# Kernel tuning notes

Hardware: AMD Instinct MI355X
Metric: run time of the kernel (lower is better)

The kernel has to match this reference:

```python
import jax, jax.numpy as jnp
import numpy as np

N_NODES = 50000
SEQ_LEN = 32
N_TOKENS = 100000
EMB_DIM = 128          # in_feats / 2
IN_FEATS = 256
N_HIDDEN = 256
N_CLASSES = 40
N_EDGES = 800000
PAD_IX = 0


def setup_inputs() -> dict:
    key = jax.random.key(0)
    k1, k2, k3, k4, k5, k6 = jax.random.split(key, 6)
    features = jax.random.randint(k1, (N_NODES, SEQ_LEN), 0, N_TOKENS, dtype=jnp.int32)
    src = jax.random.randint(k2, (N_EDGES,), 0, N_NODES, dtype=jnp.int32)
    dst = jax.random.randint(k3, (N_EDGES,), 0, N_NODES, dtype=jnp.int32)
    emb_table = jax.random.normal(k4, (N_TOKENS, EMB_DIM), dtype=jnp.float32) * 0.02
    W1 = jax.random.normal(k5, (IN_FEATS, N_HIDDEN), dtype=jnp.float32) * 0.02
    b1 = jnp.zeros((N_HIDDEN,), dtype=jnp.float32)
    W2 = jax.random.normal(k6, (N_HIDDEN, N_CLASSES), dtype=jnp.float32) * 0.02
    b2 = jnp.zeros((N_CLASSES,), dtype=jnp.float32)
    return {"features": features, "src": src, "dst": dst,
            "emb_table": emb_table, "W1": W1, "b1": b1, "W2": W2, "b2": b2}


def _apply_embs(features, emb_table):
    # padding_idx row contributes zeros (nn.Embedding padding_idx semantics)
    emb = emb_table.at[PAD_IX].set(0.0)
    h = emb[features]                                    # [N, L, D]
    seq_len = jnp.sum(features != PAD_IX, axis=1)        # [N]
    seq_len = jnp.maximum(seq_len, 1)[:, None].astype(h.dtype)
    h1 = h.sum(axis=1) / seq_len                         # masked mean
    h2 = h.max(axis=1)                                   # max pool (pads are 0)
    return jnp.concatenate((h1, h2), axis=1)             # [N, 2D]


def _graph_conv(h, src, dst, norm_s, norm_d, W, b):
    # DGL GraphConv, norm='both': out = D_in^{-1/2} A D_out^{-1/2} h W + b
    hw = h @ W                                           # transform first (smaller msgs)
    m = (hw * norm_s[:, None])[src]                      # gather messages [E, F]
    agg = jax.ops.segment_sum(m, dst, num_segments=N_NODES)
    return agg * norm_d[:, None] + b


def reference(features, src, dst, emb_table, W1, b1, W2, b2):
    ones_e = jnp.ones((src.shape[0],), dtype=jnp.float32)
    deg_out = jnp.maximum(jax.ops.segment_sum(ones_e, src, num_segments=N_NODES), 1.0)
    deg_in = jnp.maximum(jax.ops.segment_sum(ones_e, dst, num_segments=N_NODES), 1.0)
    norm_s = deg_out ** -0.5
    norm_d = deg_in ** -0.5

    h = _apply_embs(features, emb_table)                 # [N, in_feats]
    h = jax.nn.relu(_graph_conv(h, src, dst, norm_s, norm_d, W1, b1))
    # dropout is identity in eval mode
    h = _graph_conv(h, src, dst, norm_s, norm_d, W2, b2)
    return h                                             # [N, n_classes]
```

## Files before the change

kernel.cpp:

```cpp
#include <hip/hip_runtime.h>
#include <math.h>

#define N_NODES 50000
#define SEQ_LEN 32
#define EMB_DIM 128
#define IN_FEATS 256
#define N_HIDDEN 256
#define N_CLASSES 40
#define N_EDGES 800000
#define N_TOKENS 100000

#define SLOT 64
#define NBIN 196
#define BINCAP 4608
#define EPB 4000

typedef short short8 __attribute__((ext_vector_type(8)));
typedef float f32x4 __attribute__((ext_vector_type(4)));

__device__ __forceinline__ unsigned short f2bf(float x) {
  unsigned int u = __float_as_uint(x);
  unsigned int r = (u + 0x7FFFu + ((u >> 16) & 1u)) >> 16;
  return (unsigned short)r;
}
__device__ __forceinline__ float bf2f(unsigned short s) {
  return __uint_as_float((unsigned int)s << 16);
}
__device__ __forceinline__ unsigned int pack2bf(float a, float b) {
  return (unsigned int)f2bf(a) | ((unsigned int)f2bf(b) << 16);
}

__global__ __launch_bounds__(256) void k_pre(const int* __restrict__ src,
                                             const int* __restrict__ dst,
                                             int* __restrict__ gcntD,
                                             int* __restrict__ gcntS,
                                             unsigned int* __restrict__ dbin,
                                             unsigned char* __restrict__ sbin,
                                             const float* __restrict__ emb,
                                             unsigned short* __restrict__ emb_b,
                                             const float* __restrict__ W1,
                                             unsigned short* __restrict__ Wp1,
                                             const float* __restrict__ W2,
                                             unsigned short* __restrict__ Wp2) {
  __shared__ int cntD[NBIN], cntS[NBIN], baseD[NBIN], baseS[NBIN];
  int b = blockIdx.x, tid = threadIdx.x;
  if (b < 200) {
    if (tid < NBIN) { cntD[tid] = 0; cntS[tid] = 0; }
    __syncthreads();
    int e0 = b * EPB;
    for (int j = tid; j < EPB; j += 256) {
      int d = dst[e0 + j], s = src[e0 + j];
      atomicAdd(&cntD[d >> 8], 1);
      atomicAdd(&cntS[s >> 8], 1);
    }
    __syncthreads();
    if (tid < NBIN) {
      baseD[tid] = atomicAdd(&gcntD[tid], cntD[tid]);
      baseS[tid] = atomicAdd(&gcntS[tid], cntS[tid]);
      cntD[tid] = 0;
      cntS[tid] = 0;
    }
    __syncthreads();
    for (int j = tid; j < EPB; j += 256) {
      int d = dst[e0 + j], s = src[e0 + j];
      int bd = d >> 8, bs = s >> 8;
      int od = atomicAdd(&cntD[bd], 1);
      int pd = baseD[bd] + od;
      if (pd < BINCAP) dbin[(size_t)bd * BINCAP + pd] = ((unsigned int)s << 8) | (unsigned int)(d & 255);
      int os = atomicAdd(&cntS[bs], 1);
      int ps = baseS[bs] + os;
      if (ps < BINCAP) sbin[(size_t)bs * BINCAP + ps] = (unsigned char)(s & 255);
    }
  } else if (b < 200 + 2048) {
    const int total = N_TOKENS * EMB_DIM / 4;
    for (int i = (b - 200) * 256 + tid; i < total; i += 2048 * 256) {
      float4 v = ((const float4*)emb)[i];
      ushort4 o;
      o.x = f2bf(v.x); o.y = f2bf(v.y); o.z = f2bf(v.z); o.w = f2bf(v.w);
      ((ushort4*)emb_b)[i] = o;
    }
  } else if (b < 200 + 2048 + 32) {
    int g = (b - 2248) * 256 + tid;
    int lane = g & 63, jb = (g >> 6) & 15, kt = g >> 10;
    int col = jb * 16 + (lane & 15);
    int kbase = kt * 32 + (lane >> 4) * 8;
    unsigned short* o = Wp1 + (size_t)g * 8;
    #pragma unroll
    for (int e = 0; e < 8; ++e) o[e] = f2bf(W1[(size_t)(kbase + e) * N_HIDDEN + col]);
  } else {
    int g = (b - 2280) * 256 + tid;
    if (g < 8 * 3 * 64) {
      int lane = g & 63, jb = (g >> 6) % 3, kt = g / (3 * 64);
      int col = jb * 16 + (lane & 15);
      int kbase = kt * 32 + (lane >> 4) * 8;
      unsigned short* o = Wp2 + (size_t)g * 8;
      #pragma unroll
      for (int e = 0; e < 8; ++e)
        o[e] = (col < N_CLASSES) ? f2bf(W2[(size_t)(kbase + e) * N_CLASSES + col]) : (unsigned short)0;
    }
  }
}

__global__ __launch_bounds__(256) void k_graph2(const unsigned int* __restrict__ dbin,
                                                const int* __restrict__ gcntD,
                                                const unsigned char* __restrict__ sbin,
                                                const int* __restrict__ gcntS,
                                                int* __restrict__ cursor,
                                                int* __restrict__ csr_pad,
                                                float* __restrict__ norm_s,
                                                float* __restrict__ norm_d) {
  __shared__ int cntD[256], cntS[256];
  int tid = threadIdx.x, b = blockIdx.x;
  cntD[tid] = 0; cntS[tid] = 0;
  __syncthreads();
  int n = min(gcntD[b], BINCAP);
  const unsigned int* bb = dbin + (size_t)b * BINCAP;
  for (int j = tid; j < n; j += 256) {
    unsigned int e = bb[j];
    int lo = e & 255;
    int slot = atomicAdd(&cntD[lo], 1);
    if (slot < SLOT) csr_pad[(size_t)(b * 256 + lo) * SLOT + slot] = (int)(e >> 8);
  }
  int ns = min(gcntS[b], BINCAP);
  const unsigned char* sb = sbin + (size_t)b * BINCAP;
  for (int j = tid; j < ns; j += 256) atomicAdd(&cntS[sb[j]], 1);
  __syncthreads();
  int node = b * 256 + tid;
  if (node < N_NODES) {
    cursor[node] = min(cntD[tid], SLOT);
    norm_d[node] = 1.0f / sqrtf((float)max(cntD[tid], 1));
    norm_s[node] = 1.0f / sqrtf((float)max(cntS[tid], 1));
  }
}

__global__ __launch_bounds__(512) void k_emb_mm1(const int* __restrict__ feats,
                                                 const uint4* __restrict__ rows4,
                                                 const unsigned short* __restrict__ Wp,
                                                 unsigned short* __restrict__ out) {
  __shared__ unsigned short sA[64 * 256];
  int tid = threadIdx.x;
  int w = tid >> 6, lane = tid & 63;
  int r0 = blockIdx.x * 64;
  int lq = lane & 15, qg = lane >> 4, laneL = lane & 31;

  #pragma unroll
  for (int n = 0; n < 8; ++n) {
    int r = w * 8 + n;
    int node = r0 + r;
    int tok0 = 0;
    if (node < N_NODES) tok0 = feats[(size_t)node * SEQ_LEN + laneL];
    unsigned long long m = __ballot(tok0 != 0);
    int cnt = (int)__popcll(m & 0xFFFFFFFFull);
    float inv = 1.0f / (float)max(cnt, 1);

    float s0 = 0.f, s1 = 0.f, s2 = 0.f, s3 = 0.f, s4 = 0.f, s5 = 0.f, s6 = 0.f, s7 = 0.f;
    float m0 = 0.f, m1 = 0.f, m2 = 0.f, m3 = 0.f, m4 = 0.f, m5 = 0.f, m6 = 0.f, m7 = 0.f;
    bool first = true;
    #pragma unroll
    for (int t = 0; t < 8; ++t) {
      int tok = __shfl(tok0, t * 4 + qg);
      uint4 v = make_uint4(0u, 0u, 0u, 0u);
      if (tok) v = rows4[(size_t)tok * 16 + lq];
      float f0 = bf2f((unsigned short)(v.x & 0xFFFF)), f1 = bf2f((unsigned short)(v.x >> 16));
      float f2 = bf2f((unsigned short)(v.y & 0xFFFF)), f3 = bf2f((unsigned short)(v.y >> 16));
      float f4 = bf2f((unsigned short)(v.z & 0xFFFF)), f5 = bf2f((unsigned short)(v.z >> 16));
      float f6 = bf2f((unsigned short)(v.w & 0xFFFF)), f7 = bf2f((unsigned short)(v.w >> 16));
      s0 += f0; s1 += f1; s2 += f2; s3 += f3; s4 += f4; s5 += f5; s6 += f6; s7 += f7;
      if (first) { m0 = f0; m1 = f1; m2 = f2; m3 = f3; m4 = f4; m5 = f5; m6 = f6; m7 = f7; first = false; }
      else {
        m0 = fmaxf(m0, f0); m1 = fmaxf(m1, f1); m2 = fmaxf(m2, f2); m3 = fmaxf(m3, f3);
        m4 = fmaxf(m4, f4); m5 = fmaxf(m5, f5); m6 = fmaxf(m6, f6); m7 = fmaxf(m7, f7);
      }
    }
    #pragma unroll
    for (int mask = 16; mask <= 32; mask <<= 1) {
      s0 += __shfl_xor(s0, mask); s1 += __shfl_xor(s1, mask);
      s2 += __shfl_xor(s2, mask); s3 += __shfl_xor(s3, mask);
      s4 += __shfl_xor(s4, mask); s5 += __shfl_xor(s5, mask);
      s6 += __shfl_xor(s6, mask); s7 += __shfl_xor(s7, mask);
      m0 = fmaxf(m0, __shfl_xor(m0, mask)); m1 = fmaxf(m1, __shfl_xor(m1, mask));
      m2 = fmaxf(m2, __shfl_xor(m2, mask)); m3 = fmaxf(m3, __shfl_xor(m3, mask));
      m4 = fmaxf(m4, __shfl_xor(m4, mask)); m5 = fmaxf(m5, __shfl_xor(m5, mask));
      m6 = fmaxf(m6, __shfl_xor(m6, mask)); m7 = fmaxf(m7, __shfl_xor(m7, mask));
    }
    if (qg == 0) {
      int kb1 = lq, kb2 = 16 + lq;
      *(uint4*)&sA[r * 256 + ((kb1 ^ (r & 7)) << 3)] =
          make_uint4(pack2bf(s0 * inv, s1 * inv), pack2bf(s2 * inv, s3 * inv),
                     pack2bf(s4 * inv, s5 * inv), pack2bf(s6 * inv, s7 * inv));
      *(uint4*)&sA[r * 256 + ((kb2 ^ (r & 7)) << 3)] =
          make_uint4(pack2bf(m0, m1), pack2bf(m2, m3), pack2bf(m4, m5), pack2bf(m6, m7));
    }
  }
  __syncthreads();

  const short8* W8 = (const short8*)Wp;
  f32x4 acc[4][2];
  #pragma unroll
  for (int i = 0; i < 4; ++i) { acc[i][0] = (f32x4){0.f,0.f,0.f,0.f}; acc[i][1] = (f32x4){0.f,0.f,0.f,0.f}; }

  #pragma unroll
  for (int kt = 0; kt < 8; ++kt) {
    short8 a[4];
    int kb = kt * 4 + (lane >> 4);
    #pragma unroll
    for (int ri = 0; ri < 4; ++ri) {
      int r = ri * 16 + (lane & 15);
      a[ri] = *(const short8*)&sA[r * 256 + ((kb ^ (r & 7)) << 3)];
    }
    short8 b0 = W8[(kt * 16 + w * 2 + 0) * 64 + lane];
    short8 b1 = W8[(kt * 16 + w * 2 + 1) * 64 + lane];
    #pragma unroll
    for (int ri = 0; ri < 4; ++ri) {
      acc[ri][0] = __builtin_amdgcn_mfma_f32_16x16x32_bf16(a[ri], b0, acc[ri][0], 0, 0, 0);
      acc[ri][1] = __builtin_amdgcn_mfma_f32_16x16x32_bf16(a[ri], b1, acc[ri][1], 0, 0, 0);
    }
  }

  #pragma unroll
  for (int ri = 0; ri < 4; ++ri) {
    #pragma unroll
    for (int rr = 0; rr < 4; ++rr) {
      int row = r0 + ri * 16 + (lane >> 4) * 4 + rr;
      if (row < N_NODES) {
        #pragma unroll
        for (int jb = 0; jb < 2; ++jb) {
          int col = w * 32 + jb * 16 + (lane & 15);
          out[(size_t)row * 256 + col] = f2bf(acc[ri][jb][rr]);
        }
      }
    }
  }
}

__global__ __launch_bounds__(512) void k_agg_mm2(const uint4* __restrict__ rows4,
                                                 const int* __restrict__ cursor,
                                                 const int* __restrict__ csr_pad,
                                                 const float* __restrict__ norm_s,
                                                 const float* __restrict__ norm_d,
                                                 const float* __restrict__ b1,
                                                 const unsigned short* __restrict__ Wp,
                                                 unsigned short* __restrict__ out) {
  __shared__ unsigned short sA[64 * 256];
  int tid = threadIdx.x;
  int w = tid >> 6, lane = tid & 63;
  int r0 = blockIdx.x * 64;
  int half = lane >> 5, lq = lane & 31;

  #pragma unroll
  for (int n = 0; n < 8; ++n) {
    int r = w * 8 + n;
    int node = r0 + r;
    float a0 = 0.f, a1 = 0.f, a2 = 0.f, a3 = 0.f, a4 = 0.f, a5 = 0.f, a6 = 0.f, a7 = 0.f;
    if (node < N_NODES) {
      int cnt = __builtin_amdgcn_readfirstlane(cursor[node]);
      const int* csr = csr_pad + (size_t)node * SLOT;
      int e = 0;
      for (; e + 8 <= cnt; e += 8) {
        int s0 = csr[e + 0 + half], s1 = csr[e + 2 + half];
        int s2 = csr[e + 4 + half], s3 = csr[e + 6 + half];
        float ns0 = norm_s[s0], ns1 = norm_s[s1], ns2 = norm_s[s2], ns3 = norm_s[s3];
        uint4 v0 = rows4[(size_t)s0 * 32 + lq];
        uint4 v1 = rows4[(size_t)s1 * 32 + lq];
        uint4 v2 = rows4[(size_t)s2 * 32 + lq];
        uint4 v3 = rows4[(size_t)s3 * 32 + lq];
        #pragma unroll
        for (int i = 0; i < 4; ++i) {
          uint4 v = (i == 0) ? v0 : (i == 1) ? v1 : (i == 2) ? v2 : v3;
          float ns = (i == 0) ? ns0 : (i == 1) ? ns1 : (i == 2) ? ns2 : ns3;
          a0 += ns * bf2f((unsigned short)(v.x & 0xFFFF)); a1 += ns * bf2f((unsigned short)(v.x >> 16));
          a2 += ns * bf2f((unsigned short)(v.y & 0xFFFF)); a3 += ns * bf2f((unsigned short)(v.y >> 16));
          a4 += ns * bf2f((unsigned short)(v.z & 0xFFFF)); a5 += ns * bf2f((unsigned short)(v.z >> 16));
          a6 += ns * bf2f((unsigned short)(v.w & 0xFFFF)); a7 += ns * bf2f((unsigned short)(v.w >> 16));
        }
      }
      for (; e + 2 <= cnt; e += 2) {
        int s = csr[e + half];
        float ns = norm_s[s];
        uint4 v = rows4[(size_t)s * 32 + lq];
        a0 += ns * bf2f((unsigned short)(v.x & 0xFFFF)); a1 += ns * bf2f((unsigned short)(v.x >> 16));
        a2 += ns * bf2f((unsigned short)(v.y & 0xFFFF)); a3 += ns * bf2f((unsigned short)(v.y >> 16));
        a4 += ns * bf2f((unsigned short)(v.z & 0xFFFF)); a5 += ns * bf2f((unsigned short)(v.z >> 16));
        a6 += ns * bf2f((unsigned short)(v.w & 0xFFFF)); a7 += ns * bf2f((unsigned short)(v.w >> 16));
      }
      if (e < cnt && half == 0) {
        int s = csr[e];
        float ns = norm_s[s];
        uint4 v = rows4[(size_t)s * 32 + lq];
        a0 += ns * bf2f((unsigned short)(v.x & 0xFFFF)); a1 += ns * bf2f((unsigned short)(v.x >> 16));
        a2 += ns * bf2f((unsigned short)(v.y & 0xFFFF)); a3 += ns * bf2f((unsigned short)(v.y >> 16));
        a4 += ns * bf2f((unsigned short)(v.z & 0xFFFF)); a5 += ns * bf2f((unsigned short)(v.z >> 16));
        a6 += ns * bf2f((unsigned short)(v.w & 0xFFFF)); a7 += ns * bf2f((unsigned short)(v.w >> 16));
      }
    }
    a0 += __shfl_xor(a0, 32); a1 += __shfl_xor(a1, 32);
    a2 += __shfl_xor(a2, 32); a3 += __shfl_xor(a3, 32);
    a4 += __shfl_xor(a4, 32); a5 += __shfl_xor(a5, 32);
    a6 += __shfl_xor(a6, 32); a7 += __shfl_xor(a7, 32);

    if (half == 0) {
      float nd = (node < N_NODES) ? norm_d[node] : 1.0f;
      float4 bb0 = *(const float4*)&b1[8 * lq];
      float4 bb1 = *(const float4*)&b1[8 * lq + 4];
      float o0 = fmaxf(a0 * nd + bb0.x, 0.f), o1 = fmaxf(a1 * nd + bb0.y, 0.f);
      float o2 = fmaxf(a2 * nd + bb0.z, 0.f), o3 = fmaxf(a3 * nd + bb0.w, 0.f);
      float o4 = fmaxf(a4 * nd + bb1.x, 0.f), o5 = fmaxf(a5 * nd + bb1.y, 0.f);
      float o6 = fmaxf(a6 * nd + bb1.z, 0.f), o7 = fmaxf(a7 * nd + bb1.w, 0.f);
      *(uint4*)&sA[r * 256 + ((lq ^ (r & 7)) << 3)] =
          make_uint4(pack2bf(o0, o1), pack2bf(o2, o3), pack2bf(o4, o5), pack2bf(o6, o7));
    }
  }
  __syncthreads();

  if (w < 4) {
    const short8* W8 = (const short8*)Wp;
    f32x4 acc[3];
    #pragma unroll
    for (int j = 0; j < 3; ++j) acc[j] = (f32x4){0.f, 0.f, 0.f, 0.f};
    #pragma unroll
    for (int kt = 0; kt < 8; ++kt) {
      int r = w * 16 + (lane & 15);
      int kb = kt * 4 + (lane >> 4);
      short8 a = *(const short8*)&sA[r * 256 + ((kb ^ (r & 7)) << 3)];
      #pragma unroll
      for (int jb = 0; jb < 3; ++jb) {
        short8 b = W8[(kt * 3 + jb) * 64 + lane];
        acc[jb] = __builtin_amdgcn_mfma_f32_16x16x32_bf16(a, b, acc[jb], 0, 0, 0);
      }
    }
    #pragma unroll
    for (int rr = 0; rr < 4; ++rr) {
      int row = r0 + w * 16 + (lane >> 4) * 4 + rr;
      if (row < N_NODES) {
        float ns = norm_s[row];
        #pragma unroll
        for (int jb = 0; jb < 3; ++jb) {
          int col = jb * 16 + (lane & 15);
          if (col < N_CLASSES) out[(size_t)row * N_CLASSES + col] = f2bf(acc[jb][rr] * ns);
        }
      }
    }
  }
}

__global__ __launch_bounds__(256) void k_agg2(const unsigned int* __restrict__ rows,
                                              const int* __restrict__ cursor,
                                              const int* __restrict__ csr_pad,
                                              const float* __restrict__ norm_d,
                                              const float* __restrict__ b2,
                                              float* __restrict__ out) {
  int tid = threadIdx.x;
  int w = tid >> 6, lane = tid & 63;
  int node = blockIdx.x * 4 + w;
  int slot = lane / 20, fl = lane % 20;
  int cnt = __builtin_amdgcn_readfirstlane(cursor[node]);
  const int* csr = csr_pad + (size_t)node * SLOT;

  float a0 = 0.f, a1 = 0.f;
  if (slot < 3) {
    for (int e = slot; e < cnt; e += 3) {
      int s = csr[e];
      unsigned int v = rows[(size_t)s * 20 + fl];
      a0 += bf2f((unsigned short)(v & 0xFFFF));
      a1 += bf2f((unsigned short)(v >> 16));
    }
  }
  float p0 = __shfl(a0, lane + 20), p1 = __shfl(a1, lane + 20);
  float q0 = __shfl(a0, lane + 40), q1 = __shfl(a1, lane + 40);
  if (slot == 0) {
    a0 += p0 + q0; a1 += p1 + q1;
    float nd = norm_d[node];
    float o0 = a0 * nd + b2[2 * fl];
    float o1 = a1 * nd + b2[2 * fl + 1];
    *(float2*)&out[(size_t)node * N_CLASSES + 2 * fl] = make_float2(o0, o1);
  }
}

extern "C" void kernel_launch(void* const* d_in, const int* in_sizes, int n_in,
                              void* d_out, int out_size, void* d_ws, size_t ws_size,
                              hipStream_t stream) {
  const int*   feats = (const int*)d_in[0];
  const int*   src   = (const int*)d_in[1];
  const int*   dst   = (const int*)d_in[2];
  const float* emb   = (const float*)d_in[3];
  const float* W1    = (const float*)d_in[4];
  const float* b1    = (const float*)d_in[5];
  const float* W2    = (const float*)d_in[6];
  const float* b2    = (const float*)d_in[7];
  float* out = (float*)d_out;

  char* base = (char*)d_ws;
  size_t off = 0;
  auto alloc = [&](size_t bytes) -> char* {
    char* p = base + off;
    off += (bytes + 255) & ~(size_t)255;
    return p;
  };
  unsigned short* msgb    = (unsigned short*)alloc((size_t)N_NODES * N_HIDDEN * 2);
  unsigned short* hw2b    = (unsigned short*)alloc((size_t)N_NODES * N_CLASSES * 2);
  unsigned short* emb_b   = (unsigned short*)alloc((size_t)N_TOKENS * EMB_DIM * 2);
  unsigned short* Wp1     = (unsigned short*)alloc((size_t)8 * 16 * 64 * 8 * 2);
  unsigned short* Wp2     = (unsigned short*)alloc((size_t)8 * 3 * 64 * 8 * 2);
  int*   gcnt    = (int*)alloc((size_t)512 * 4);
  int*   gcntD   = gcnt;
  int*   gcntS   = gcnt + 256;
  int*   cursor  = (int*)alloc((size_t)N_NODES * 4);
  float* norm_s  = (float*)alloc((size_t)N_NODES * 4);
  float* norm_d  = (float*)alloc((size_t)N_NODES * 4);
  unsigned int*  dbin = (unsigned int*)alloc((size_t)NBIN * BINCAP * 4);
  unsigned char* sbin = (unsigned char*)alloc((size_t)NBIN * BINCAP);
  int*   csr_pad = (int*)alloc((size_t)N_NODES * SLOT * 4);

  hipMemsetAsync(gcnt, 0, 512 * 4, stream);

  k_pre<<<200 + 2048 + 32 + 6, 256, 0, stream>>>(src, dst, gcntD, gcntS, dbin, sbin,
                                                 emb, emb_b, W1, Wp1, W2, Wp2);
  k_graph2<<<NBIN, 256, 0, stream>>>(dbin, gcntD, sbin, gcntS, cursor, csr_pad, norm_s, norm_d);

  int gemm_blocks = (N_NODES + 63) / 64;
  k_emb_mm1<<<gemm_blocks, 512, 0, stream>>>(feats, (const uint4*)emb_b, Wp1, msgb);
  k_agg_mm2<<<gemm_blocks, 512, 0, stream>>>((const uint4*)msgb, cursor, csr_pad,
                                             norm_s, norm_d, b1, Wp2, hw2b);
  k_agg2<<<N_NODES / 4, 256, 0, stream>>>((const unsigned int*)hw2b, cursor, csr_pad, norm_d, b2, out);
}
```

Measured before the change: 230.8 us.

## Split fused aggregation+GEMM2 into separate kernels and fold norm_s into GEMM1 output

The source-degree normalization moves out of the first aggregation's gather loop and into the epilogue of the first GEMM, so the aggregation no longer does a dependent norm_s lookup per edge. The fused agg+mm2 kernel is split into a one-wave-per-node aggregation kernel that writes the hidden layer to a new bf16 buffer, then a separate GEMM kernel that reads it back. The second aggregation is also widened to 6 edge slots with 8-byte loads per lane. The trade is an extra 25 MB write and read of the hidden activations plus one more launch, in exchange for better occupancy and load balance in the gather.

```diff
diff --git a/kernel.cpp b/kernel.cpp
--- a/kernel.cpp
+++ b/kernel.cpp
@@ -136,6 +136,7 @@
 __global__ __launch_bounds__(512) void k_emb_mm1(const int* __restrict__ feats,
                                                  const uint4* __restrict__ rows4,
                                                  const unsigned short* __restrict__ Wp,
+                                                 const float* __restrict__ norm_s,
                                                  unsigned short* __restrict__ out) {
   __shared__ unsigned short sA[64 * 256];
   int tid = threadIdx.x;
@@ -223,127 +224,133 @@
     for (int rr = 0; rr < 4; ++rr) {
       int row = r0 + ri * 16 + (lane >> 4) * 4 + rr;
       if (row < N_NODES) {
+        float ns = norm_s[row];
         #pragma unroll
         for (int jb = 0; jb < 2; ++jb) {
           int col = w * 32 + jb * 16 + (lane & 15);
-          out[(size_t)row * 256 + col] = f2bf(acc[ri][jb][rr]);
+          out[(size_t)row * 256 + col] = f2bf(acc[ri][jb][rr] * ns);
         }
       }
     }
   }
 }
 
-__global__ __launch_bounds__(512) void k_agg_mm2(const uint4* __restrict__ rows4,
-                                                 const int* __restrict__ cursor,
-                                                 const int* __restrict__ csr_pad,
-                                                 const float* __restrict__ norm_s,
-                                                 const float* __restrict__ norm_d,
-                                                 const float* __restrict__ b1,
-                                                 const unsigned short* __restrict__ Wp,
-                                                 unsigned short* __restrict__ out) {
+__global__ __launch_bounds__(256) void k_agg1(const uint4* __restrict__ rows4,
+                                              const int* __restrict__ cursor,
+                                              const int* __restrict__ csr_pad,
+                                              const float* __restrict__ norm_d,
+                                              const float* __restrict__ b1,
+                                              uint4* __restrict__ out4) {
+  int tid = threadIdx.x;
+  int w = tid >> 6, lane = tid & 63;
+  int node = blockIdx.x * 4 + w;
+  int cnt = __builtin_amdgcn_readfirstlane(cursor[node]);
+  const int* csr = csr_pad + (size_t)node * SLOT;
+  int half = lane >> 5, lq = lane & 31;
+
+  float a0 = 0.f, a1 = 0.f, a2 = 0.f, a3 = 0.f, a4 = 0.f, a5 = 0.f, a6 = 0.f, a7 = 0.f;
+  int e = 0;
+  for (; e + 8 <= cnt; e += 8) {
+    int s0 = csr[e + 0 + half], s1 = csr[e + 2 + half];
+    int s2 = csr[e + 4 + half], s3 = csr[e + 6 + half];
+    uint4 v0 = rows4[(size_t)s0 * 32 + lq];
+    uint4 v1 = rows4[(size_t)s1 * 32 + lq];
+    uint4 v2 = rows4[(size_t)s2 * 32 + lq];
+    uint4 v3 = rows4[(size_t)s3 * 32 + lq];
+    #pragma unroll
+    for (int i = 0; i < 4; ++i) {
+      uint4 v = (i == 0) ? v0 : (i == 1) ? v1 : (i == 2) ? v2 : v3;
+      a0 += bf2f((unsigned short)(v.x & 0xFFFF)); a1 += bf2f((unsigned short)(v.x >> 16));
+      a2 += bf2f((unsigned short)(v.y & 0xFFFF)); a3 += bf2f((unsigned short)(v.y >> 16));
+      a4 += bf2f((unsigned short)(v.z & 0xFFFF)); a5 += bf2f((unsigned short)(v.z >> 16));
+      a6 += bf2f((unsigned short)(v.w & 0xFFFF)); a7 += bf2f((unsigned short)(v.w >> 16));
+    }
+  }
+  for (; e + 2 <= cnt; e += 2) {
+    int s = csr[e + half];
+    uint4 v = rows4[(size_t)s * 32 + lq];
+    a0 += bf2f((unsigned short)(v.x & 0xFFFF)); a1 += bf2f((unsigned short)(v.x >> 16));
+    a2 += bf2f((unsigned short)(v.y & 0xFFFF)); a3 += bf2f((unsigned short)(v.y >> 16));
+    a4 += bf2f((unsigned short)(v.z & 0xFFFF)); a5 += bf2f((unsigned short)(v.z >> 16));
+    a6 += bf2f((unsigned short)(v.w & 0xFFFF)); a7 += bf2f((unsigned short)(v.w >> 16));
+  }
+  if (e < cnt) {
+    uint4 v = make_uint4(0u, 0u, 0u, 0u);
+    if (half == 0) v = rows4[(size_t)csr[e] * 32 + lq];
+    a0 += bf2f((unsigned short)(v.x & 0xFFFF)); a1 += bf2f((unsigned short)(v.x >> 16));
+    a2 += bf2f((unsigned short)(v.y & 0xFFFF)); a3 += bf2f((unsigned short)(v.y >> 16));
+    a4 += bf2f((unsigned short)(v.z & 0xFFFF)); a5 += bf2f((unsigned short)(v.z >> 16));
+    a6 += bf2f((unsigned short)(v.w & 0xFFFF)); a7 += bf2f((unsigned short)(v.w >> 16));
+  }
+  a0 += __shfl_xor(a0, 32); a1 += __shfl_xor(a1, 32);
+  a2 += __shfl_xor(a2, 32); a3 += __shfl_xor(a3, 32);
+  a4 += __shfl_xor(a4, 32); a5 += __shfl_xor(a5, 32);
+  a6 += __shfl_xor(a6, 32); a7 += __shfl_xor(a7, 32);
+
+  if (half == 0) {
+    float nd = norm_d[node];
+    float4 bb0 = *(const float4*)&b1[8 * lq];
+    float4 bb1 = *(const float4*)&b1[8 * lq + 4];
+    float o0 = fmaxf(a0 * nd + bb0.x, 0.f), o1 = fmaxf(a1 * nd + bb0.y, 0.f);
+    float o2 = fmaxf(a2 * nd + bb0.z, 0.f), o3 = fmaxf(a3 * nd + bb0.w, 0.f);
+    float o4 = fmaxf(a4 * nd + bb1.x, 0.f), o5 = fmaxf(a5 * nd + bb1.y, 0.f);
+    float o6 = fmaxf(a6 * nd + bb1.z, 0.f), o7 = fmaxf(a7 * nd + bb1.w, 0.f);
+    out4[(size_t)node * 32 + lq] = make_uint4(pack2bf(o0, o1), pack2bf(o2, o3),
+                                              pack2bf(o4, o5), pack2bf(o6, o7));
+  }
+}
+
+__global__ __launch_bounds__(256) void k_mm2(const unsigned short* __restrict__ h2b,
+                                             const unsigned short* __restrict__ Wp,
+                                             const float* __restrict__ norm_s,
+                                             unsigned short* __restrict__ out) {
   __shared__ unsigned short sA[64 * 256];
   int tid = threadIdx.x;
+  int r0 = blockIdx.x * 64;
+  #pragma unroll
+  for (int it = 0; it < 8; ++it) {
+    int idx = it * 256 + tid;
+    int r = idx >> 5, kb = idx & 31;
+    uint4 v = make_uint4(0, 0, 0, 0);
+    int row = r0 + r;
+    if (row < N_NODES) v = *(const uint4*)(h2b + (size_t)row * 256 + kb * 8);
+    *(uint4*)&sA[r * 256 + ((kb ^ (r & 7)) << 3)] = v;
+  }
+  __syncthreads();
+
   int w = tid >> 6, lane = tid & 63;
-  int r0 = blockIdx.x * 64;
-  int half = lane >> 5, lq = lane & 31;
-
-  #pragma unroll
-  for (int n = 0; n < 8; ++n) {
-    int r = w * 8 + n;
-    int node = r0 + r;
-    float a0 = 0.f, a1 = 0.f, a2 = 0.f, a3 = 0.f, a4 = 0.f, a5 = 0.f, a6 = 0.f, a7 = 0.f;
-    if (node < N_NODES) {
-      int cnt = __builtin_amdgcn_readfirstlane(cursor[node]);
-      const int* csr = csr_pad + (size_t)node * SLOT;
-      int e = 0;
-      for (; e + 8 <= cnt; e += 8) {
-        int s0 = csr[e + 0 + half], s1 = csr[e + 2 + half];
-        int s2 = csr[e + 4 + half], s3 = csr[e + 6 + half];
-        float ns0 = norm_s[s0], ns1 = norm_s[s1], ns2 = norm_s[s2], ns3 = norm_s[s3];
-        uint4 v0 = rows4[(size_t)s0 * 32 + lq];
-        uint4 v1 = rows4[(size_t)s1 * 32 + lq];
-        uint4 v2 = rows4[(size_t)s2 * 32 + lq];
-        uint4 v3 = rows4[(size_t)s3 * 32 + lq];
-        #pragma unroll
-        for (int i = 0; i < 4; ++i) {
-          uint4 v = (i == 0) ? v0 : (i == 1) ? v1 : (i == 2) ? v2 : v3;
-          float ns = (i == 0) ? ns0 : (i == 1) ? ns1 : (i == 2) ? ns2 : ns3;
-          a0 += ns * bf2f((unsigned short)(v.x & 0xFFFF)); a1 += ns * bf2f((unsigned short)(v.x >> 16));
-          a2 += ns * bf2f((unsigned short)(v.y & 0xFFFF)); a3 += ns * bf2f((unsigned short)(v.y >> 16));
-          a4 += ns * bf2f((unsigned short)(v.z & 0xFFFF)); a5 += ns * bf2f((unsigned short)(v.z >> 16));
-          a6 += ns * bf2f((unsigned short)(v.w & 0xFFFF)); a7 += ns * bf2f((unsigned short)(v.w >> 16));
-        }
-      }
-      for (; e + 2 <= cnt; e += 2) {
-        int s = csr[e + half];
-        float ns = norm_s[s];
-        uint4 v = rows4[(size_t)s * 32 + lq];
-        a0 += ns * bf2f((unsigned short)(v.x & 0xFFFF)); a1 += ns * bf2f((unsigned short)(v.x >> 16));
-        a2 += ns * bf2f((unsigned short)(v.y & 0xFFFF)); a3 += ns * bf2f((unsigned short)(v.y >> 16));
-        a4 += ns * bf2f((unsigned short)(v.z & 0xFFFF)); a5 += ns * bf2f((unsigned short)(v.z >> 16));
-        a6 += ns * bf2f((unsigned short)(v.w & 0xFFFF)); a7 += ns * bf2f((unsigned short)(v.w >> 16));
-      }
-      if (e < cnt && half == 0) {
-        int s = csr[e];
-        float ns = norm_s[s];
-        uint4 v = rows4[(size_t)s * 32 + lq];
-        a0 += ns * bf2f((unsigned short)(v.x & 0xFFFF)); a1 += ns * bf2f((unsigned short)(v.x >> 16));
-        a2 += ns * bf2f((unsigned short)(v.y & 0xFFFF)); a3 += ns * bf2f((unsigned short)(v.y >> 16));
-        a4 += ns * bf2f((unsigned short)(v.z & 0xFFFF)); a5 += ns * bf2f((unsigned short)(v.z >> 16));
-        a6 += ns * bf2f((unsigned short)(v.w & 0xFFFF)); a7 += ns * bf2f((unsigned short)(v.w >> 16));
-      }
-    }
-    a0 += __shfl_xor(a0, 32); a1 += __shfl_xor(a1, 32);
-    a2 += __shfl_xor(a2, 32); a3 += __shfl_xor(a3, 32);
-    a4 += __shfl_xor(a4, 32); a5 += __shfl_xor(a5, 32);
-    a6 += __shfl_xor(a6, 32); a7 += __shfl_xor(a7, 32);
-
-    if (half == 0) {
-      float nd = (node < N_NODES) ? norm_d[node] : 1.0f;
-      float4 bb0 = *(const float4*)&b1[8 * lq];
-      float4 bb1 = *(const float4*)&b1[8 * lq + 4];
-      float o0 = fmaxf(a0 * nd + bb0.x, 0.f), o1 = fmaxf(a1 * nd + bb0.y, 0.f);
-      float o2 = fmaxf(a2 * nd + bb0.z, 0.f), o3 = fmaxf(a3 * nd + bb0.w, 0.f);
-      float o4 = fmaxf(a4 * nd + bb1.x, 0.f), o5 = fmaxf(a5 * nd + bb1.y, 0.f);
-      float o6 = fmaxf(a6 * nd + bb1.z, 0.f), o7 = fmaxf(a7 * nd + bb1.w, 0.f);
-      *(uint4*)&sA[r * 256 + ((lq ^ (r & 7)) << 3)] =
-          make_uint4(pack2bf(o0, o1), pack2bf(o2, o3), pack2bf(o4, o5), pack2bf(o6, o7));
-    }
-  }
-  __syncthreads();
-
-  if (w < 4) {
-    const short8* W8 = (const short8*)Wp;
-    f32x4 acc[3];
-    #pragma unroll
-    for (int j = 0; j < 3; ++j) acc[j] = (f32x4){0.f, 0.f, 0.f, 0.f};
-    #pragma unroll
-    for (int kt = 0; kt < 8; ++kt) {
-      int r = w * 16 + (lane & 15);
-      int kb = kt * 4 + (lane >> 4);
-      short8 a = *(const short8*)&sA[r * 256 + ((kb ^ (r & 7)) << 3)];
+  const short8* W8 = (const short8*)Wp;
+  f32x4 acc[3];
+  #pragma unroll
+  for (int j = 0; j < 3; ++j) acc[j] = (f32x4){0.f, 0.f, 0.f, 0.f};
+
+  #pragma unroll
+  for (int kt = 0; kt < 8; ++kt) {
+    int r = w * 16 + (lane & 15);
+    int kb = kt * 4 + (lane >> 4);
+    short8 a = *(const short8*)&sA[r * 256 + ((kb ^ (r & 7)) << 3)];
+    #pragma unroll
+    for (int jb = 0; jb < 3; ++jb) {
+      short8 b = W8[(kt * 3 + jb) * 64 + lane];
+      acc[jb] = __builtin_amdgcn_mfma_f32_16x16x32_bf16(a, b, acc[jb], 0, 0, 0);
+    }
+  }
+
+  #pragma unroll
+  for (int rr = 0; rr < 4; ++rr) {
+    int row = r0 + w * 16 + (lane >> 4) * 4 + rr;
+    if (row < N_NODES) {
+      float ns = norm_s[row];
       #pragma unroll
       for (int jb = 0; jb < 3; ++jb) {
-        short8 b = W8[(kt * 3 + jb) * 64 + lane];
-        acc[jb] = __builtin_amdgcn_mfma_f32_16x16x32_bf16(a, b, acc[jb], 0, 0, 0);
+        int col = jb * 16 + (lane & 15);
+        if (col < N_CLASSES) out[(size_t)row * N_CLASSES + col] = f2bf(acc[jb][rr] * ns);
       }
     }
-    #pragma unroll
-    for (int rr = 0; rr < 4; ++rr) {
-      int row = r0 + w * 16 + (lane >> 4) * 4 + rr;
-      if (row < N_NODES) {
-        float ns = norm_s[row];
-        #pragma unroll
-        for (int jb = 0; jb < 3; ++jb) {
-          int col = jb * 16 + (lane & 15);
-          if (col < N_CLASSES) out[(size_t)row * N_CLASSES + col] = f2bf(acc[jb][rr] * ns);
-        }
-      }
-    }
-  }
-}
-
-__global__ __launch_bounds__(256) void k_agg2(const unsigned int* __restrict__ rows,
+  }
+}
+
+__global__ __launch_bounds__(256) void k_agg2(const uint2* __restrict__ rows2,
                                               const int* __restrict__ cursor,
                                               const int* __restrict__ csr_pad,
                                               const float* __restrict__ norm_d,
@@ -352,27 +359,35 @@
   int tid = threadIdx.x;
   int w = tid >> 6, lane = tid & 63;
   int node = blockIdx.x * 4 + w;
-  int slot = lane / 20, fl = lane % 20;
+  int slot = lane / 10, fl = lane % 10;
   int cnt = __builtin_amdgcn_readfirstlane(cursor[node]);
   const int* csr = csr_pad + (size_t)node * SLOT;
 
-  float a0 = 0.f, a1 = 0.f;
-  if (slot < 3) {
-    for (int e = slot; e < cnt; e += 3) {
+  float a0 = 0.f, a1 = 0.f, a2 = 0.f, a3 = 0.f;
+  if (slot < 6) {
+    for (int e = slot; e < cnt; e += 6) {
       int s = csr[e];
-      unsigned int v = rows[(size_t)s * 20 + fl];
-      a0 += bf2f((unsigned short)(v & 0xFFFF));
-      a1 += bf2f((unsigned short)(v >> 16));
-    }
-  }
-  float p0 = __shfl(a0, lane + 20), p1 = __shfl(a1, lane + 20);
-  float q0 = __shfl(a0, lane + 40), q1 = __shfl(a1, lane + 40);
+      uint2 v = rows2[(size_t)s * 10 + fl];
+      a0 += bf2f((unsigned short)(v.x & 0xFFFF));
+      a1 += bf2f((unsigned short)(v.x >> 16));
+      a2 += bf2f((unsigned short)(v.y & 0xFFFF));
+      a3 += bf2f((unsigned short)(v.y >> 16));
+    }
+  }
+  float r10_0 = __shfl(a0, lane + 10), r10_1 = __shfl(a1, lane + 10), r10_2 = __shfl(a2, lane + 10), r10_3 = __shfl(a3, lane + 10);
+  float r20_0 = __shfl(a0, lane + 20), r20_1 = __shfl(a1, lane + 20), r20_2 = __shfl(a2, lane + 20), r20_3 = __shfl(a3, lane + 20);
+  float r30_0 = __shfl(a0, lane + 30), r30_1 = __shfl(a1, lane + 30), r30_2 = __shfl(a2, lane + 30), r30_3 = __shfl(a3, lane + 30);
+  float r40_0 = __shfl(a0, lane + 40), r40_1 = __shfl(a1, lane + 40), r40_2 = __shfl(a2, lane + 40), r40_3 = __shfl(a3, lane + 40);
+  float r50_0 = __shfl(a0, lane + 50), r50_1 = __shfl(a1, lane + 50), r50_2 = __shfl(a2, lane + 50), r50_3 = __shfl(a3, lane + 50);
   if (slot == 0) {
-    a0 += p0 + q0; a1 += p1 + q1;
+    a0 += r10_0 + r20_0 + r30_0 + r40_0 + r50_0;
+    a1 += r10_1 + r20_1 + r30_1 + r40_1 + r50_1;
+    a2 += r10_2 + r20_2 + r30_2 + r40_2 + r50_2;
+    a3 += r10_3 + r20_3 + r30_3 + r40_3 + r50_3;
     float nd = norm_d[node];
-    float o0 = a0 * nd + b2[2 * fl];
-    float o1 = a1 * nd + b2[2 * fl + 1];
-    *(float2*)&out[(size_t)node * N_CLASSES + 2 * fl] = make_float2(o0, o1);
+    float4 bb = *(const float4*)&b2[4 * fl];
+    float4 o = make_float4(a0 * nd + bb.x, a1 * nd + bb.y, a2 * nd + bb.z, a3 * nd + bb.w);
+    *(float4*)&out[(size_t)node * N_CLASSES + 4 * fl] = o;
   }
 }
 
@@ -396,6 +411,7 @@
     off += (bytes + 255) & ~(size_t)255;
     return p;
   };
+  unsigned short* hb      = (unsigned short*)alloc((size_t)N_NODES * N_HIDDEN * 2);
   unsigned short* msgb    = (unsigned short*)alloc((size_t)N_NODES * N_HIDDEN * 2);
   unsigned short* hw2b    = (unsigned short*)alloc((size_t)N_NODES * N_CLASSES * 2);
   unsigned short* emb_b   = (unsigned short*)alloc((size_t)N_TOKENS * EMB_DIM * 2);
@@ -418,8 +434,8 @@
   k_graph2<<<NBIN, 256, 0, stream>>>(dbin, gcntD, sbin, gcntS, cursor, csr_pad, norm_s, norm_d);
 
   int gemm_blocks = (N_NODES + 63) / 64;
-  k_emb_mm1<<<gemm_blocks, 512, 0, stream>>>(feats, (const uint4*)emb_b, Wp1, msgb);
-  k_agg_mm2<<<gemm_blocks, 512, 0, stream>>>((const uint4*)msgb, cursor, csr_pad,
-                                             norm_s, norm_d, b1, Wp2, hw2b);
-  k_agg2<<<N_NODES / 4, 256, 0, stream>>>((const unsigned int*)hw2b, cursor, csr_pad, norm_d, b2, out);
-}
+  k_emb_mm1<<<gemm_blocks, 512, 0, stream>>>(feats, (const uint4*)emb_b, Wp1, norm_s, msgb);
+  k_agg1<<<N_NODES / 4, 256, 0, stream>>>((const uint4*)msgb, cursor, csr_pad, norm_d, b1, (uint4*)hb);
+  k_mm2<<<gemm_blocks, 256, 0, stream>>>(hb, Wp2, norm_s, hw2b);
+  k_agg2<<<N_NODES / 4, 256, 0, stream>>>((const uint2*)hw2b, cursor, csr_pad, norm_d, b2, out);
+}
```

Result: faster. 212.3 us (-8.0%).
